# Optimization experiments

Measured on AMD Instinct MI355X. Metric: run time of the kernel, lower is better.

The kernel has to match this reference:

```python
import jax, jax.numpy as jnp
import numpy as np

THETA = 10000.0

def _rope(x, pos):
    # x: [b, h, s, hd]; pos: [s]
    hd = x.shape[-1]
    inv_freq = 1.0 / (THETA ** (jnp.arange(0, hd, 2, dtype=jnp.float32) / hd))  # [hd/2]
    ang = pos.astype(jnp.float32)[:, None] * inv_freq[None, :]                   # [s, hd/2]
    cos, sin = jnp.cos(ang), jnp.sin(ang)
    x1, x2 = x[..., 0::2], x[..., 1::2]
    r1 = x1 * cos - x2 * sin
    r2 = x1 * sin + x2 * cos
    return jnp.stack([r1, r2], axis=-1).reshape(x.shape)

def setup_inputs() -> dict:
    key = jax.random.key(0)
    ks = jax.random.split(key, 5)
    b, s, d = 2, 2048, 1024
    scale = 0.02
    return {
        "x": jax.random.normal(ks[0], (b, s, d), dtype=jnp.float32),
        "Wq": jax.random.normal(ks[1], (d, d), dtype=jnp.float32) * scale,
        "Wk": jax.random.normal(ks[2], (d, d), dtype=jnp.float32) * scale,
        "Wv": jax.random.normal(ks[3], (d, d), dtype=jnp.float32) * scale,
        "Wo": jax.random.normal(ks[4], (d, d), dtype=jnp.float32) * scale,
    }

def reference(x, Wq, Wk, Wv, Wo):
    b, s, d = x.shape
    n_heads = 16
    hd = d // n_heads

    def split_heads(t):  # [b,s,d] -> [b,h,s,hd]
        return t.reshape(b, s, n_heads, hd).transpose(0, 2, 1, 3)

    q = split_heads(x @ Wq.T)
    k = split_heads(x @ Wk.T)
    v = split_heads(x @ Wv.T)

    pos = jnp.arange(s)
    q = _rope(q, pos)
    k = _rope(k, pos)

    scores = jnp.einsum("bhqd,bhkd->bhqk", q, k) / jnp.sqrt(jnp.float32(hd))
    causal = jnp.tril(jnp.ones((s, s), dtype=bool))
    scores = jnp.where(causal, scores, -jnp.inf)
    attn = jax.nn.softmax(scores, axis=-1)
    ctx = jnp.einsum("bhqk,bhkd->bhqd", attn, v)
    ctx = ctx.transpose(0, 2, 1, 3).reshape(b, s, d)
    return ctx @ Wo.T
```

## Files before the change

### kernel.cpp

```cpp
#include <hip/hip_runtime.h>
#include <math.h>

#define B  2
#define S  2048
#define D  1024
#define NH 16
#define HD 64
#define NROWS (B * S)

#define AS1 __attribute__((address_space(1)))
#define AS3 __attribute__((address_space(3)))
#define GLD16(g, l) __builtin_amdgcn_global_load_lds((const AS1 void*)(g), (AS3 void*)(l), 16, 0, 0)

typedef __attribute__((ext_vector_type(8))) short short8;
typedef __attribute__((ext_vector_type(4))) float floatx4;

#define MFMA16(a, b, c) __builtin_amdgcn_mfma_f32_16x16x32_bf16((a), (b), (c), 0, 0, 0)

__device__ inline float fexp2(float x) { return __builtin_amdgcn_exp2f(x); }

__device__ inline unsigned short f2bf(float f) {
    union { float f; unsigned int u; } v; v.f = f;
    unsigned int u = v.u;
    u += 0x7fffu + ((u >> 16) & 1);
    return (unsigned short)(u >> 16);
}

__device__ inline unsigned int pack2bf(float a, float b) {
    unsigned int ua = __float_as_uint(a) + 0x8000u;
    unsigned int ub = __float_as_uint(b) + 0x8000u;
    return __builtin_amdgcn_perm(ub, ua, 0x07060302u);
}

__global__ __launch_bounds__(256) void cvt_kernel(
    const float* __restrict__ x,  const float* __restrict__ Wq,
    const float* __restrict__ Wk, const float* __restrict__ Wv,
    const float* __restrict__ Wo,
    unsigned short* __restrict__ xb,  unsigned short* __restrict__ wqb,
    unsigned short* __restrict__ wkb, unsigned short* __restrict__ wvb,
    unsigned short* __restrict__ wob, float2* __restrict__ tab)
{
    size_t idx = (size_t)blockIdx.x * 256 + threadIdx.x;
    if (idx >= (2u << 20)) {
        int tt = (int)(idx - (2u << 20));
        int j  = tt >> 9;
        int s0 = (tt & 511) << 2;
        float invf = fexp2(-(float)j * (13.287712379549449f / 32.0f));
        #pragma unroll
        for (int p = 0; p < 4; ++p) {
            float sn, cs;
            __sincosf((float)(s0 + p) * invf, &sn, &cs);
            tab[j * 2048 + s0 + p] = make_float2(cs, sn);
        }
        return;
    }
    const float* src; unsigned short* dst; size_t off;
    if (idx < (1u << 20)) { src = x; dst = xb; off = idx << 2; }
    else {
        size_t r = idx - (1u << 20);
        int w = (int)(r >> 18);
        off = (r & ((1u << 18) - 1)) << 2;
        src = (w == 0) ? Wq : (w == 1) ? Wk : (w == 2) ? Wv : Wo;
        dst = (w == 0) ? wqb : (w == 1) ? wkb : (w == 2) ? wvb : wob;
    }
    float4 f = *(const float4*)(src + off);
    ushort4 o;
    o.x = f2bf(f.x); o.y = f2bf(f.y); o.z = f2bf(f.z); o.w = f2bf(f.w);
    *(ushort4*)(dst + off) = o;
}

#define G2STAGE(Abase, Bbase, kk, AD, BD)                                      \
{                                                                              \
    GLD16(Abase + (size_t)rowS        * D + (kk) + koS, AD + t * 8);           \
    GLD16(Abase + (size_t)(rowS + 64) * D + (kk) + koS, AD + 2048 + t * 8);    \
    GLD16(Bbase + (size_t)rowS        * D + (kk) + koS, BD + t * 8);           \
    GLD16(Bbase + (size_t)(rowS + 64) * D + (kk) + koS, BD + 2048 + t * 8);    \
}

#define G2COMP(AC, BC)                                                         \
{                                                                              \
    short8 a[4], b[4];                                                         \
    _Pragma("unroll")                                                          \
    for (int mi = 0; mi < 4; ++mi)                                             \
        a[mi] = *(const short8*)&AC[(wr * 64 + mi * 16 + lm) * 32 + quad * 8]; \
    _Pragma("unroll")                                                          \
    for (int ni = 0; ni < 4; ++ni)                                             \
        b[ni] = *(const short8*)&BC[(wc * 64 + ni * 16 + lm) * 32 + quad * 8]; \
    _Pragma("unroll")                                                          \
    for (int mi = 0; mi < 4; ++mi)                                             \
        _Pragma("unroll")                                                      \
        for (int ni = 0; ni < 4; ++ni)                                         \
            acc[mi][ni] = MFMA16(b[ni], a[mi], acc[mi][ni]);      \
}

__global__ __launch_bounds__(256, 3) void gemm_qkv_mfma(
    const unsigned short* __restrict__ xb,
    const unsigned short* __restrict__ wqb,
    const unsigned short* __restrict__ wkb,
    const unsigned short* __restrict__ wvb,
    const float2* __restrict__ tab,
    unsigned short* __restrict__ Qo, unsigned short* __restrict__ Ko,
    unsigned short* __restrict__ Vo)
{
    __shared__ short As0[128 * 32];
    __shared__ short As1[128 * 32];
    __shared__ short Bs0[128 * 32];
    __shared__ short Bs1[128 * 32];

    const int t    = threadIdx.x;
    const int wave = t >> 6, lane = t & 63;
    const int lm   = lane & 15, quad = lane >> 4;
    const int wr   = wave >> 1, wc = wave & 1;
    const int rowS = t >> 2;
    const int koS  = (t & 3) << 3;

    const int i0  = blockIdx.x * 128;
    const int by  = blockIdx.y;
    const int mat = by >> 3;
    const int j0  = (by & 7) * 128;
    const unsigned short* __restrict__ W = (mat == 0) ? wqb : (mat == 1) ? wkb : wvb;
    unsigned short* __restrict__ out = (mat == 0) ? Qo : (mat == 1) ? Ko : Vo;

    const unsigned short* Abase = xb + (size_t)i0 * D;
    const unsigned short* Bbase = W  + (size_t)j0 * D;

    floatx4 acc[4][4] = {};

    G2STAGE(Abase, Bbase, 0, As0, Bs0);
    __syncthreads();
    for (int k0 = 0; k0 < D; k0 += 64) {
        G2STAGE(Abase, Bbase, k0 + 32, As1, Bs1);
        G2COMP(As0, Bs0);
        __syncthreads();
        if (k0 + 64 < D) G2STAGE(Abase, Bbase, k0 + 64, As0, Bs0);
        G2COMP(As1, Bs1);
        __syncthreads();
    }

    const int h = (j0 + wc * 64) >> 6;
    if (mat < 2) {
        #pragma unroll
        for (int mi = 0; mi < 4; ++mi) {
            const int mg = i0 + wr * 64 + mi * 16 + lm;
            const int si = mg & (S - 1), bb = mg >> 11;
            unsigned short* orow = out + ((size_t)(bb * NH + h) * S + si) * HD;
            #pragma unroll
            for (int ni = 0; ni < 4; ++ni) {
                const int dim0 = ni * 16 + quad * 4;
                const int j = dim0 >> 1;
                float2 t0 = tab[j * 2048 + si];
                float2 t1 = tab[(j + 1) * 2048 + si];
                floatx4 v = acc[mi][ni];
                float r0 = v[0] * t0.x - v[1] * t0.y;
                float r1 = v[0] * t0.y + v[1] * t0.x;
                float r2 = v[2] * t1.x - v[3] * t1.y;
                float r3 = v[2] * t1.y + v[3] * t1.x;
                if (mat == 0) {
                    r0 *= 0.1803368801111204f; r1 *= 0.1803368801111204f;
                    r2 *= 0.1803368801111204f; r3 *= 0.1803368801111204f;
                }
                ushort4 pk;
                pk.x = f2bf(r0); pk.y = f2bf(r1);
                pk.z = f2bf(r2); pk.w = f2bf(r3);
                *(ushort4*)(orow + dim0) = pk;
            }
        }
    } else {
        #pragma unroll
        for (int mi = 0; mi < 4; ++mi) {
            const int mg = i0 + wr * 64 + mi * 16 + lm;
            const int si = mg & (S - 1), bb = mg >> 11;
            unsigned short* vb = out + (size_t)(bb * NH + h) * HD * S + si;
            #pragma unroll
            for (int ni = 0; ni < 4; ++ni) {
                const int d0 = ni * 16 + quad * 4;
                #pragma unroll
                for (int p = 0; p < 4; ++p)
                    vb[(size_t)(d0 + p) * S] = f2bf(acc[mi][ni][p]);
            }
        }
    }
}

#define GSTAGE(Abase, Bbase, kk, AD, BD)                                       \
{                                                                              \
    GLD16(Abase + (size_t)rowA  * D + (kk) + koA,  AD + cA  * 8);              \
    GLD16(Bbase + (size_t)rowB0 * D + (kk) + koB0, BD + cB0 * 8);              \
    GLD16(Bbase + (size_t)rowB1 * D + (kk) + koB1, BD + cB1 * 8);              \
}

#define GCOMP(AC, BC)                                                          \
{                                                                              \
    short8 a[4], b[2];                                                         \
    _Pragma("unroll")                                                          \
    for (int mi = 0; mi < 4; ++mi)                                             \
        a[mi] = *(const short8*)&AC[(mi * 16 + lm) * 32 + quad * 8];           \
    _Pragma("unroll")                                                          \
    for (int ni = 0; ni < 2; ++ni)                                             \
        b[ni] = *(const short8*)&BC[(wave * 32 + ni * 16 + lm) * 32 + quad * 8]; \
    _Pragma("unroll")                                                          \
    for (int mi = 0; mi < 4; ++mi)                                             \
        _Pragma("unroll")                                                      \
        for (int ni = 0; ni < 2; ++ni)                                         \
            acc[mi][ni] = MFMA16(b[ni], a[mi], acc[mi][ni]);      \
}

#define GEMM_PREAMBLE                                                          \
    const int t    = threadIdx.x;                                              \
    const int wave = t >> 6, lane = t & 63;                                    \
    const int lm   = lane & 15, quad = lane >> 4;                              \
    const int cA   = wave * 64 + lane;                                         \
    const int rowA = cA >> 2,  koA  = (cA & 3) << 3;                           \
    const int cB0  = wave * 128 + lane;                                        \
    const int rowB0 = cB0 >> 2, koB0 = (cB0 & 3) << 3;                         \
    const int cB1  = cB0 + 64;                                                 \
    const int rowB1 = cB1 >> 2, koB1 = (cB1 & 3) << 3;

#define GEMM_KLOOP(Abase, Bbase)                                               \
    GSTAGE(Abase, Bbase, 0, As0, Bs0);                                         \
    __syncthreads();                                                           \
    for (int k0 = 0; k0 < D; k0 += 64) {                                       \
        GSTAGE(Abase, Bbase, k0 + 32, As1, Bs1);                               \
        GCOMP(As0, Bs0);                                                       \
        __syncthreads();                                                       \
        if (k0 + 64 < D) GSTAGE(Abase, Bbase, k0 + 64, As0, Bs0);              \
        GCOMP(As1, Bs1);                                                       \
        __syncthreads();                                                       \
    }

__global__ __launch_bounds__(256) void gemm_out_mfma(
    const unsigned short* __restrict__ Cb,
    const unsigned short* __restrict__ wob,
    float* __restrict__ out)
{
    __shared__ short As0[64 * 32];
    __shared__ short As1[64 * 32];
    __shared__ short Bs0[128 * 32];
    __shared__ short Bs1[128 * 32];

    GEMM_PREAMBLE
    const int i0 = blockIdx.x * 64;
    const int j0 = blockIdx.y * 128;

    const unsigned short* Abase = Cb  + (size_t)i0 * D;
    const unsigned short* Bbase = wob + (size_t)j0 * D;

    floatx4 acc[4][2] = {};
    GEMM_KLOOP(Abase, Bbase)

    #pragma unroll
    for (int mi = 0; mi < 4; ++mi) {
        const int mg = i0 + mi * 16 + lm;
        float* orow = out + (size_t)mg * D;
        #pragma unroll
        for (int ni = 0; ni < 2; ++ni) {
            const int ng = j0 + wave * 32 + ni * 16 + quad * 4;
            *(floatx4*)(orow + ng) = acc[mi][ni];
        }
    }
}

__global__ __launch_bounds__(512, 4) void attn_mfma(
    const unsigned short* __restrict__ Qb,
    const unsigned short* __restrict__ Kb,
    const unsigned short* __restrict__ Vt,
    unsigned short* __restrict__ Cb)
{
    __shared__ unsigned short Ks[2][64][64];
    __shared__ unsigned short Vs[2][64][64];
    __shared__ unsigned short Ps[128][64];

    const int t    = threadIdx.x;
    const int lane = t & 63, wave = t >> 6;
    const int lm   = lane & 15, quad = lane >> 4;
    const int sw   = lm & 7;
    const int psw  = (lm & 7) << 1;

    const int b     = blockIdx.x;
    const int bh    = b & 31;
    const int f     = (b >> 5) & 7;
    const int round = b >> 8;
    const int qt    = (round == 0) ? f : 15 - f;
    const int q0    = qt * 128;
    const int nkv   = 2 * qt + 2;
    const int myNkv = 2 * qt + 1 + (wave >> 2);

    const unsigned short* Qg = Qb + (size_t)bh * S * HD;
    const unsigned short* Kg = Kb + (size_t)bh * S * HD;
    const unsigned short* Vg = Vt + (size_t)bh * HD * S;

    short8 qa0 = *(const short8*)(Qg + (size_t)(q0 + 16 * wave + lm) * HD + quad * 8);
    short8 qa1 = *(const short8*)(Qg + (size_t)(q0 + 16 * wave + lm) * HD + 32 + quad * 8);

    short8 vones;
    #pragma unroll
    for (int i = 0; i < 8; ++i) vones[i] = (short)0x3F80;

    const int srow = t >> 3;
    const int sch  = (t & 7) ^ (srow & 7);

    GLD16(Kg + (size_t)srow * HD + sch * 8,        &Ks[0][0][0] + t * 8);
    GLD16(Vg + (size_t)srow * S + sch * 8,         &Vs[0][0][0] + t * 8);
    GLD16(Kg + (size_t)(64 + srow) * HD + sch * 8, &Ks[1][0][0] + t * 8);

    floatx4 o[4] = {};
    floatx4 osum = {};
    floatx4 sc[4], scn[4];
    #pragma unroll
    for (int nt = 0; nt < 4; ++nt) scn[nt] = floatx4{0.f, 0.f, 0.f, 0.f};

    __syncthreads();

    #pragma unroll
    for (int nt = 0; nt < 4; ++nt) {
        short8 kb0 = *(const short8*)&Ks[0][nt * 16 + lm][(quad ^ sw) * 8];
        short8 kb1 = *(const short8*)&Ks[0][nt * 16 + lm][((4 + quad) ^ sw) * 8];
        floatx4 s = {0.f, 0.f, 0.f, 0.f};
        s = MFMA16(kb0, qa0, s);
        s = MFMA16(kb1, qa1, s);
        sc[nt] = s;
    }

    __syncthreads();

    for (int kt = 0; kt < nkv; ++kt) {
        const int pb = kt & 1;

        if (kt + 2 < nkv)
            GLD16(Kg + (size_t)((kt + 2) * 64 + srow) * HD + sch * 8,
                  &Ks[pb][0][0] + t * 8);
        if (kt + 1 < nkv)
            GLD16(Vg + (size_t)srow * S + (kt + 1) * 64 + sch * 8,
                  &Vs[pb ^ 1][0][0] + t * 8);

        if (kt < myNkv) {
            if (kt == myNkv - 1) {
                const int rel = q0 + 16 * wave + lm - kt * 64;
                #pragma unroll
                for (int nt = 0; nt < 4; ++nt)
                    #pragma unroll
                    for (int r = 0; r < 4; ++r) {
                        float pe = fexp2(sc[nt][r]);
                        if (nt * 16 + quad * 4 + r > rel) pe = 0.0f;
                        sc[nt][r] = pe;
                    }
            } else {
                #pragma unroll
                for (int nt = 0; nt < 4; ++nt)
                    #pragma unroll
                    for (int r = 0; r < 4; ++r)
                        sc[nt][r] = fexp2(sc[nt][r]);
            }

            #pragma unroll
            for (int nt = 0; nt < 4; ++nt) {
                uint2 pk;
                pk.x = pack2bf(sc[nt][0], sc[nt][1]);
                pk.y = pack2bf(sc[nt][2], sc[nt][3]);
                int cp = (nt * 4 + quad) ^ psw;
                *(uint2*)&Ps[16 * wave + lm][cp * 4] = pk;
            }

            if (kt + 1 < myNkv) {
                #pragma unroll
                for (int nt = 0; nt < 4; ++nt) {
                    short8 kb0 = *(const short8*)&Ks[pb ^ 1][nt * 16 + lm][(quad ^ sw) * 8];
                    short8 kb1 = *(const short8*)&Ks[pb ^ 1][nt * 16 + lm][((4 + quad) ^ sw) * 8];
                    floatx4 s = {0.f, 0.f, 0.f, 0.f};
                    s = MFMA16(kb0, qa0, s);
                    s = MFMA16(kb1, qa1, s);
                    scn[nt] = s;
                }
            }

            short8 pa0 = *(const short8*)&Ps[16 * wave + lm][((quad * 2) ^ psw) * 4];
            short8 pa1 = *(const short8*)&Ps[16 * wave + lm][((8 + quad * 2) ^ psw) * 4];
            osum = MFMA16(pa0, vones, osum);
            osum = MFMA16(pa1, vones, osum);
            #pragma unroll
            for (int nt = 0; nt < 4; ++nt) {
                short8 vb0 = *(const short8*)&Vs[pb][nt * 16 + lm][(quad ^ sw) * 8];
                short8 vb1 = *(const short8*)&Vs[pb][nt * 16 + lm][((4 + quad) ^ sw) * 8];
                o[nt] = MFMA16(pa0, vb0, o[nt]);
                o[nt] = MFMA16(pa1, vb1, o[nt]);
            }
        }

        __syncthreads();

        if (kt + 1 < myNkv) {
            #pragma unroll
            for (int nt = 0; nt < 4; ++nt) sc[nt] = scn[nt];
        }
    }

    const int h = bh & (NH - 1), bb = bh >> 4;
    #pragma unroll
    for (int r = 0; r < 4; ++r) {
        float inv = 1.0f / osum[r];
        size_t row = (size_t)bb * S + q0 + 16 * wave + quad * 4 + r;
        #pragma unroll
        for (int nt = 0; nt < 4; ++nt)
            Cb[row * D + h * HD + nt * 16 + lm] = f2bf(o[nt][r] * inv);
    }
}

extern "C" void kernel_launch(void* const* d_in, const int* in_sizes, int n_in,
                              void* d_out, int out_size, void* d_ws, size_t ws_size,
                              hipStream_t stream) {
    (void)in_sizes; (void)n_in; (void)out_size; (void)ws_size;
    const float* x  = (const float*)d_in[0];
    const float* Wq = (const float*)d_in[1];
    const float* Wk = (const float*)d_in[2];
    const float* Wv = (const float*)d_in[3];
    const float* Wo = (const float*)d_in[4];
    float* out = (float*)d_out;

    char* w = (char*)d_ws;
    unsigned short* Qb  = (unsigned short*)(w);
    unsigned short* Kb  = (unsigned short*)(w + (((size_t)8)  << 20));
    unsigned short* Vtb = (unsigned short*)(w + (((size_t)16) << 20));
    unsigned short* Cb  = (unsigned short*)(w + (((size_t)24) << 20));
    unsigned short* xb  = (unsigned short*)(w + (((size_t)32) << 20));
    unsigned short* wqb = (unsigned short*)(w + (((size_t)40) << 20));
    unsigned short* wkb = (unsigned short*)(w + (((size_t)42) << 20));
    unsigned short* wvb = (unsigned short*)(w + (((size_t)44) << 20));
    unsigned short* wob = (unsigned short*)(w + (((size_t)46) << 20));
    float2*         tab = (float2*)(w + (((size_t)48) << 20));

    cvt_kernel<<<8256, 256, 0, stream>>>(x, Wq, Wk, Wv, Wo,
                                         xb, wqb, wkb, wvb, wob, tab);

    dim3 g1(NROWS / 128, 24);
    gemm_qkv_mfma<<<g1, 256, 0, stream>>>(xb, wqb, wkb, wvb, tab, Qb, Kb, Vtb);

    attn_mfma<<<512, 512, 0, stream>>>(Qb, Kb, Vtb, Cb);

    dim3 g3(NROWS / 64, D / 128);
    gemm_out_mfma<<<g3, 256, 0, stream>>>(Cb, wob, out);
}
```

Baseline: 168.3 us.

## Fuse Q/K/V projections per head into one block sharing the x tile

Each block of the QKV GEMM now computes all three projections for one head (64 columns each of Wq, Wk, Wv) over a 128-row x tile, instead of a 128x128 tile of a single matrix. The x tile is loaded once and reused across Q, K and V, which cuts redundant A-operand traffic and shrinks the grid from 24 to 16 column blocks. It uses more LDS and accumulator registers, so launch bounds drop from 3 to 2 blocks per CU, which may reduce occupancy and latency hiding.

```diff
diff --git a/kernel.cpp b/kernel.cpp
--- a/kernel.cpp
+++ b/kernel.cpp
@@ -69,31 +69,38 @@
     *(ushort4*)(dst + off) = o;
 }
 
-#define G2STAGE(Abase, Bbase, kk, AD, BD)                                      \
+#define G3STAGE(kk, AD, QD, KD, VD)                                            \
 {                                                                              \
-    GLD16(Abase + (size_t)rowS        * D + (kk) + koS, AD + t * 8);           \
-    GLD16(Abase + (size_t)(rowS + 64) * D + (kk) + koS, AD + 2048 + t * 8);    \
-    GLD16(Bbase + (size_t)rowS        * D + (kk) + koS, BD + t * 8);           \
-    GLD16(Bbase + (size_t)(rowS + 64) * D + (kk) + koS, BD + 2048 + t * 8);    \
-}
-
-#define G2COMP(AC, BC)                                                         \
+    GLD16(Ab + (size_t)rowS        * D + (kk) + koS, AD + t * 8);              \
+    GLD16(Ab + (size_t)(rowS + 64) * D + (kk) + koS, AD + 2048 + t * 8);       \
+    GLD16(Bq + (size_t)rowS        * D + (kk) + koS, QD + t * 8);              \
+    GLD16(Bk + (size_t)rowS        * D + (kk) + koS, KD + t * 8);              \
+    GLD16(Bv + (size_t)rowS        * D + (kk) + koS, VD + t * 8);              \
+}
+
+#define G3COMP(AC, QC, KC, VC)                                                 \
 {                                                                              \
-    short8 a[4], b[4];                                                         \
+    short8 a[4], bq[2], bk[2], bv[2];                                          \
     _Pragma("unroll")                                                          \
     for (int mi = 0; mi < 4; ++mi)                                             \
         a[mi] = *(const short8*)&AC[(wr * 64 + mi * 16 + lm) * 32 + quad * 8]; \
     _Pragma("unroll")                                                          \
-    for (int ni = 0; ni < 4; ++ni)                                             \
-        b[ni] = *(const short8*)&BC[(wc * 64 + ni * 16 + lm) * 32 + quad * 8]; \
+    for (int ni = 0; ni < 2; ++ni) {                                           \
+        bq[ni] = *(const short8*)&QC[(wc * 32 + ni * 16 + lm) * 32 + quad * 8]; \
+        bk[ni] = *(const short8*)&KC[(wc * 32 + ni * 16 + lm) * 32 + quad * 8]; \
+        bv[ni] = *(const short8*)&VC[(wc * 32 + ni * 16 + lm) * 32 + quad * 8]; \
+    }                                                                          \
     _Pragma("unroll")                                                          \
     for (int mi = 0; mi < 4; ++mi)                                             \
         _Pragma("unroll")                                                      \
-        for (int ni = 0; ni < 4; ++ni)                                         \
-            acc[mi][ni] = MFMA16(b[ni], a[mi], acc[mi][ni]);      \
-}
-
-__global__ __launch_bounds__(256, 3) void gemm_qkv_mfma(
+        for (int ni = 0; ni < 2; ++ni) {                                       \
+            accQ[mi][ni] = MFMA16(bq[ni], a[mi], accQ[mi][ni]);   \
+            accK[mi][ni] = MFMA16(bk[ni], a[mi], accK[mi][ni]);                \
+            accV[mi][ni] = MFMA16(bv[ni], a[mi], accV[mi][ni]);                \
+        }                                                                      \
+}
+
+__global__ __launch_bounds__(256, 2) void gemm_qkv_mfma(
     const unsigned short* __restrict__ xb,
     const unsigned short* __restrict__ wqb,
     const unsigned short* __restrict__ wkb,
@@ -104,8 +111,12 @@
 {
     __shared__ short As0[128 * 32];
     __shared__ short As1[128 * 32];
-    __shared__ short Bs0[128 * 32];
-    __shared__ short Bs1[128 * 32];
+    __shared__ short Bqs0[64 * 32];
+    __shared__ short Bqs1[64 * 32];
+    __shared__ short Bks0[64 * 32];
+    __shared__ short Bks1[64 * 32];
+    __shared__ short Bvs0[64 * 32];
+    __shared__ short Bvs1[64 * 32];
 
     const int t    = threadIdx.x;
     const int wave = t >> 6, lane = t & 63;
@@ -114,70 +125,65 @@
     const int rowS = t >> 2;
     const int koS  = (t & 3) << 3;
 
-    const int i0  = blockIdx.x * 128;
-    const int by  = blockIdx.y;
-    const int mat = by >> 3;
-    const int j0  = (by & 7) * 128;
-    const unsigned short* __restrict__ W = (mat == 0) ? wqb : (mat == 1) ? wkb : wvb;
-    unsigned short* __restrict__ out = (mat == 0) ? Qo : (mat == 1) ? Ko : Vo;
-
-    const unsigned short* Abase = xb + (size_t)i0 * D;
-    const unsigned short* Bbase = W  + (size_t)j0 * D;
-
-    floatx4 acc[4][4] = {};
-
-    G2STAGE(Abase, Bbase, 0, As0, Bs0);
+    const int i0 = blockIdx.x * 128;
+    const int h  = blockIdx.y;
+
+    const unsigned short* Ab = xb  + (size_t)i0 * D;
+    const unsigned short* Bq = wqb + (size_t)h * 64 * D;
+    const unsigned short* Bk = wkb + (size_t)h * 64 * D;
+    const unsigned short* Bv = wvb + (size_t)h * 64 * D;
+
+    floatx4 accQ[4][2] = {}, accK[4][2] = {}, accV[4][2] = {};
+
+    G3STAGE(0, As0, Bqs0, Bks0, Bvs0);
     __syncthreads();
     for (int k0 = 0; k0 < D; k0 += 64) {
-        G2STAGE(Abase, Bbase, k0 + 32, As1, Bs1);
-        G2COMP(As0, Bs0);
+        G3STAGE(k0 + 32, As1, Bqs1, Bks1, Bvs1);
+        G3COMP(As0, Bqs0, Bks0, Bvs0);
         __syncthreads();
-        if (k0 + 64 < D) G2STAGE(Abase, Bbase, k0 + 64, As0, Bs0);
-        G2COMP(As1, Bs1);
+        if (k0 + 64 < D) G3STAGE(k0 + 64, As0, Bqs0, Bks0, Bvs0);
+        G3COMP(As1, Bqs1, Bks1, Bvs1);
         __syncthreads();
     }
 
-    const int h = (j0 + wc * 64) >> 6;
-    if (mat < 2) {
+    #pragma unroll
+    for (int mi = 0; mi < 4; ++mi) {
+        const int mg = i0 + wr * 64 + mi * 16 + lm;
+        const int si = mg & (S - 1), bb = mg >> 11;
+        unsigned short* qrow = Qo + ((size_t)(bb * NH + h) * S + si) * HD;
+        unsigned short* krow = Ko + ((size_t)(bb * NH + h) * S + si) * HD;
+        unsigned short* vb   = Vo + (size_t)(bb * NH + h) * HD * S + si;
         #pragma unroll
-        for (int mi = 0; mi < 4; ++mi) {
-            const int mg = i0 + wr * 64 + mi * 16 + lm;
-            const int si = mg & (S - 1), bb = mg >> 11;
-            unsigned short* orow = out + ((size_t)(bb * NH + h) * S + si) * HD;
-            #pragma unroll
-            for (int ni = 0; ni < 4; ++ni) {
-                const int dim0 = ni * 16 + quad * 4;
-                const int j = dim0 >> 1;
-                float2 t0 = tab[j * 2048 + si];
-                float2 t1 = tab[(j + 1) * 2048 + si];
-                floatx4 v = acc[mi][ni];
+        for (int ni = 0; ni < 2; ++ni) {
+            const int dim0 = wc * 32 + ni * 16 + quad * 4;
+            const int j = dim0 >> 1;
+            float2 t0 = tab[j * 2048 + si];
+            float2 t1 = tab[(j + 1) * 2048 + si];
+            {
+                floatx4 v = accQ[mi][ni];
+                float r0 = (v[0] * t0.x - v[1] * t0.y) * 0.1803368801111204f;
+                float r1 = (v[0] * t0.y + v[1] * t0.x) * 0.1803368801111204f;
+                float r2 = (v[2] * t1.x - v[3] * t1.y) * 0.1803368801111204f;
+                float r3 = (v[2] * t1.y + v[3] * t1.x) * 0.1803368801111204f;
+                ushort4 pk;
+                pk.x = f2bf(r0); pk.y = f2bf(r1);
+                pk.z = f2bf(r2); pk.w = f2bf(r3);
+                *(ushort4*)(qrow + dim0) = pk;
+            }
+            {
+                floatx4 v = accK[mi][ni];
                 float r0 = v[0] * t0.x - v[1] * t0.y;
                 float r1 = v[0] * t0.y + v[1] * t0.x;
                 float r2 = v[2] * t1.x - v[3] * t1.y;
                 float r3 = v[2] * t1.y + v[3] * t1.x;
-                if (mat == 0) {
-                    r0 *= 0.1803368801111204f; r1 *= 0.1803368801111204f;
-                    r2 *= 0.1803368801111204f; r3 *= 0.1803368801111204f;
-                }
                 ushort4 pk;
                 pk.x = f2bf(r0); pk.y = f2bf(r1);
                 pk.z = f2bf(r2); pk.w = f2bf(r3);
-                *(ushort4*)(orow + dim0) = pk;
-            }
-        }
-    } else {
-        #pragma unroll
-        for (int mi = 0; mi < 4; ++mi) {
-            const int mg = i0 + wr * 64 + mi * 16 + lm;
-            const int si = mg & (S - 1), bb = mg >> 11;
-            unsigned short* vb = out + (size_t)(bb * NH + h) * HD * S + si;
+                *(ushort4*)(krow + dim0) = pk;
+            }
             #pragma unroll
-            for (int ni = 0; ni < 4; ++ni) {
-                const int d0 = ni * 16 + quad * 4;
-                #pragma unroll
-                for (int p = 0; p < 4; ++p)
-                    vb[(size_t)(d0 + p) * S] = f2bf(acc[mi][ni][p]);
-            }
+            for (int p = 0; p < 4; ++p)
+                vb[(size_t)(dim0 + p) * S] = f2bf(accV[mi][ni][p]);
         }
     }
 }
@@ -431,7 +437,7 @@
     cvt_kernel<<<8256, 256, 0, stream>>>(x, Wq, Wk, Wv, Wo,
                                          xb, wqb, wkb, wvb, wob, tab);
 
-    dim3 g1(NROWS / 128, 24);
+    dim3 g1(NROWS / 128, NH);
     gemm_qkv_mfma<<<g1, 256, 0, stream>>>(xb, wqb, wkb, wvb, tab, Qb, Kb, Vtb);
 
     attn_mfma<<<512, 512, 0, stream>>>(Qb, Kb, Vtb, Cb);
```

New measurement: 168.3 us. About the same (+0.0%).
